# Performance work log

Hardware: AMD Instinct MI355X
Metric: run time of the kernel (lower is better)

## Reference

```python
import jax, jax.numpy as jnp
import numpy as np

B, S, HID = 1, 2048, 4096
NH, NKV, HD = 32, 8, 128
WINDOW = 1024
ROPE_THETA = 1e6
NEG = -1e9


def rotate_half(x):
    x1, x2 = jnp.split(x, 2, axis=-1)
    return jnp.concatenate((-x2, x1), axis=-1)


def setup_inputs() -> dict:
    key = jax.random.key(0)
    ks = jax.random.split(key, 10)
    hidden_states = jax.random.normal(ks[0], (B, S, HID), jnp.float32)
    # rotary tables [max_pos, head_dim]
    inv_freq = 1.0 / (ROPE_THETA ** (jnp.arange(0, HD, 2, dtype=jnp.float32) / HD))
    t = jnp.arange(S, dtype=jnp.float32)
    freqs = jnp.outer(t, inv_freq)                       # [S, HD/2]
    emb = jnp.concatenate((freqs, freqs), axis=-1)       # [S, HD]
    cos, sin = jnp.cos(emb), jnp.sin(emb)
    position_ids = jnp.arange(S, dtype=jnp.int64)[None, :].astype(jnp.int32)
    # sliding-window causal additive mask [B,1,S,S]
    i = jnp.arange(S)[:, None]
    j = jnp.arange(S)[None, :]
    allowed = (j <= i) & (j > i - WINDOW)
    attention_mask = jnp.where(allowed, 0.0, NEG).astype(jnp.float32)[None, None]
    sc = 0.02
    Wq = jax.random.normal(ks[1], (HID, NH * HD), jnp.float32) * sc
    bq = jax.random.normal(ks[2], (NH * HD,), jnp.float32) * sc
    Wk = jax.random.normal(ks[3], (HID, NKV * HD), jnp.float32) * sc
    bk = jax.random.normal(ks[4], (NKV * HD,), jnp.float32) * sc
    Wv = jax.random.normal(ks[5], (HID, NKV * HD), jnp.float32) * sc
    bv = jax.random.normal(ks[6], (NKV * HD,), jnp.float32) * sc
    Wo = jax.random.normal(ks[7], (NH * HD, HID), jnp.float32) * sc
    bo = jax.random.normal(ks[8], (HID,), jnp.float32) * sc
    return dict(hidden_states=hidden_states, attention_mask=attention_mask,
                position_ids=position_ids, cos=cos, sin=sin,
                Wq=Wq, bq=bq, Wk=Wk, bk=bk, Wv=Wv, bv=bv, Wo=Wo, bo=bo)


def reference(hidden_states, attention_mask, position_ids, cos, sin,
              Wq, bq, Wk, bk, Wv, bv, Wo, bo):
    bsz, q_len, _ = hidden_states.shape
    q = (hidden_states @ Wq + bq).reshape(bsz, q_len, NH, HD).transpose(0, 2, 1, 3)
    k = (hidden_states @ Wk + bk).reshape(bsz, q_len, NKV, HD).transpose(0, 2, 1, 3)
    v = (hidden_states @ Wv + bv).reshape(bsz, q_len, NKV, HD).transpose(0, 2, 1, 3)
    # RoPE: cos/sin gathered by position_ids -> [B,1,S,HD]
    c = cos[position_ids][:, None]
    s = sin[position_ids][:, None]
    q = q * c + rotate_half(q) * s
    k = k * c + rotate_half(k) * s
    # GQA repeat_kv: [B,NKV,S,HD] -> [B,NH,S,HD]
    n_rep = NH // NKV
    k = jnp.repeat(k, n_rep, axis=1)
    v = jnp.repeat(v, n_rep, axis=1)
    scores = jnp.einsum('bhqd,bhkd->bhqk', q, k) / np.sqrt(HD).astype(np.float32)
    scores = scores + attention_mask[:, :, :, :k.shape[2]]
    probs = jax.nn.softmax(scores.astype(jnp.float32), axis=-1).astype(q.dtype)
    attn = jnp.einsum('bhqk,bhkd->bhqd', probs, v)
    attn = attn.transpose(0, 2, 1, 3).reshape(bsz, q_len, NH * HD)
    return attn @ Wo + bo
```

## Files before the change

kernel.cpp:

```cpp
#include <hip/hip_runtime.h>
#include <stdint.h>

typedef unsigned short u16;
typedef __attribute__((ext_vector_type(4))) float f32x4;
typedef __attribute__((ext_vector_type(16))) float f32x16;
typedef __attribute__((ext_vector_type(8))) __bf16 bf16x8;
typedef __attribute__((ext_vector_type(4))) u16 u16x4;
typedef __attribute__((ext_vector_type(8))) u16 u16x8;
typedef __attribute__((ext_vector_type(4))) unsigned int u32x4;

#define S_LEN 2048
#define HIDDEN 4096
#define NHEAD 32
#define NKVH 8
#define HD 128
#define WIN 1024

__device__ __forceinline__ float bf2f(u16 u) {
  union { unsigned int i; float f; } x; x.i = ((unsigned int)u) << 16; return x.f;
}
__device__ __forceinline__ u16 f2bf(float f) {
  union { float f; unsigned int i; } x; x.f = f;
  unsigned int r = x.i + 0x7FFFu + ((x.i >> 16) & 1u);
  return (u16)(r >> 16);
}

__device__ __forceinline__ void gload16(const void* g, void* l) {
  __builtin_amdgcn_global_load_lds((const __attribute__((address_space(1))) void*)g,
                                   (__attribute__((address_space(3))) void*)l, 16, 0, 0);
}

__device__ __forceinline__ unsigned int cvtpk_bf16(float a, float b) {
  unsigned int w;
  asm("v_cvt_pk_bf16_f32 %0, %1, %2" : "=v"(w) : "v"(a), "v"(b));
  return w;
}

__device__ __forceinline__ void transp_f32(const float* __restrict__ in, int istride,
                                           u16* __restrict__ out, int ostride,
                                           int bx, int by, char* smem) {
  float (*tile)[68] = (float (*)[68])smem;
  int r0 = bx * 64, c0 = by * 64;
  int t = threadIdx.x;
  int tr = t >> 4;
  int tc = (t & 15) * 4;
#pragma unroll
  for (int i = 0; i < 4; ++i) {
    int r = i * 16 + tr;
    *(f32x4*)&tile[r][tc] = *(const f32x4*)(in + (size_t)(r0 + r) * istride + c0 + tc);
  }
  __syncthreads();
#pragma unroll
  for (int i = 0; i < 4; ++i) {
    int rr = i * 16 + tr;
    u16x4 o;
#pragma unroll
    for (int j = 0; j < 4; ++j) o[j] = f2bf(tile[tc + j][rr]);
    *(u16x4*)(out + (size_t)(c0 + rr) * ostride + r0 + tc) = o;
  }
}

__global__ __launch_bounds__(256) void prep_k(const float* __restrict__ X,
                                              const float* __restrict__ Wq, const float* __restrict__ Wk,
                                              const float* __restrict__ Wv,
                                              const float* __restrict__ bq, const float* __restrict__ bk,
                                              const float* __restrict__ bv,
                                              u16* __restrict__ Xb, u16* __restrict__ WT,
                                              float* __restrict__ bqkv) {
  __shared__ __align__(16) char smem[17408];
  int bid = blockIdx.x;
  if (bid < 4096) {
    size_t i = ((size_t)bid * 256 + threadIdx.x) * 8;
    f32x4 a = *(const f32x4*)(X + i);
    f32x4 b = *(const f32x4*)(X + i + 4);
    u16x8 o;
    o[0] = f2bf(a[0]); o[1] = f2bf(a[1]); o[2] = f2bf(a[2]); o[3] = f2bf(a[3]);
    o[4] = f2bf(b[0]); o[5] = f2bf(b[1]); o[6] = f2bf(b[2]); o[7] = f2bf(b[3]);
    *(u16x8*)(Xb + i) = o;
  } else if (bid < 8192) {
    int tt = bid - 4096;
    transp_f32(Wq, 4096, WT, 4096, tt & 63, tt >> 6, smem);
  } else if (bid < 9216) {
    int tt = bid - 8192;
    transp_f32(Wk, 1024, WT + (size_t)4096 * 4096, 4096, tt & 63, tt >> 6, smem);
  } else if (bid < 10240) {
    int tt = bid - 9216;
    transp_f32(Wv, 1024, WT + (size_t)5120 * 4096, 4096, tt & 63, tt >> 6, smem);
  } else {
    int i = (bid - 10240) * 256 + threadIdx.x;
    float v = (i < 4096) ? bq[i] : (i < 5120 ? bk[i - 4096] : bv[i - 5120]);
    bqkv[i] = v;
  }
}

__global__ __launch_bounds__(512, 2) void gemmqkv_k(const u16* __restrict__ A, const u16* __restrict__ Bt,
                                                    const float* __restrict__ bias,
                                                    const int* __restrict__ pos,
                                                    const float* __restrict__ cosT, const float* __restrict__ sinT,
                                                    u16* __restrict__ Q, u16* __restrict__ Kf,
                                                    u16* __restrict__ Vf, int K) {
  __shared__ __align__(16) u16 SM[49152];
  u16* SA = SM;
  u16* SB = SM + 24576;

  int tid = threadIdx.x;
  int w = tid >> 6, l = tid & 63;
  int cl = l & 15, g = l >> 4;
  int wr = w >> 2, wc = w & 3;

  int cpx = gridDim.x >> 3;
  int wg = (blockIdx.x & 7) * cpx + (blockIdx.x >> 3);
  int bm = wg & 7, bn = wg >> 3;

  const u16* Ag = A + (size_t)(bm * 256) * K;
  const u16* Bg = Bt + (size_t)(bn * 256) * K;
  int srow = w * 16 + (l >> 2);
  int csrc = ((l & 3) ^ ((l >> 3) & 3)) * 8;
  int rdc = (g ^ ((cl >> 1) & 3)) << 3;

  f32x4 acc[8][4] = {};
  int NT = K >> 5;

  auto stage = [&](int slot, int tt, int u) {
    if (u < 2) {
      gload16(Ag + (size_t)(u * 128 + srow) * K + tt * 32 + csrc,
              (void*)(SA + slot * 8192 + u * 4096 + w * 512));
    } else {
      int ub = u - 2;
      gload16(Bg + (size_t)(ub * 128 + srow) * K + tt * 32 + csrc,
              (void*)(SB + slot * 8192 + ub * 4096 + w * 512));
    }
  };

#pragma unroll
  for (int u = 0; u < 4; ++u) stage(0, 0, u);
#pragma unroll
  for (int u = 0; u < 4; ++u) stage(1, 1, u);

  for (int t = 0; t < NT; ++t) {
    asm volatile("s_waitcnt vmcnt(4)" ::: "memory");
    __builtin_amdgcn_s_barrier();
    asm volatile("" ::: "memory");

    int slot = t % 3, ss = (t + 2) % 3;
    int ts = t + 2; if (ts >= NT) ts -= NT;
#pragma unroll
    for (int u = 0; u < 4; ++u) stage(ss, ts, u);

    const u16* sa = SA + slot * 8192;
    const u16* sb = SB + slot * 8192;
    bf16x8 af[8], bf[4];
#pragma unroll
    for (int mi = 0; mi < 8; ++mi)
      af[mi] = *(const bf16x8*)(sa + (wr * 128 + mi * 16 + cl) * 32 + rdc);
#pragma unroll
    for (int ni = 0; ni < 4; ++ni)
      bf[ni] = *(const bf16x8*)(sb + (wc * 64 + ni * 16 + cl) * 32 + rdc);
    __builtin_amdgcn_s_setprio(1);
#pragma unroll
    for (int mi = 0; mi < 8; ++mi)
#pragma unroll
      for (int ni = 0; ni < 4; ++ni)
        acc[mi][ni] = __builtin_amdgcn_mfma_f32_16x16x32_bf16(af[mi], bf[ni], acc[mi][ni], 0, 0, 0);
    __builtin_amdgcn_s_setprio(0);
  }

  asm volatile("s_waitcnt vmcnt(0)" ::: "memory");
  __syncthreads();

  u16 (*tileL)[264] = (u16 (*)[264])SM;
  const float qs = 0.08838834764831845f;
#pragma unroll
  for (int hp = 0; hp < 2; ++hp) {
    if (wr == hp) {
#pragma unroll
      for (int mi = 0; mi < 8; ++mi)
#pragma unroll
        for (int ni = 0; ni < 4; ++ni) {
          int col = wc * 64 + ni * 16 + cl;
          float bb = bias[bn * 256 + col];
#pragma unroll
          for (int r = 0; r < 4; ++r)
            tileL[mi * 16 + g * 4 + r][col] = f2bf(acc[mi][ni][r] + bb);
        }
    }
    __syncthreads();

    int s0 = bm * 256 + hp * 128;
    if (bn < 16) {
      int r = tid >> 2, u2 = tid & 3;
      int hl = u2 >> 1, u = u2 & 1;
      int hq = bn * 2 + hl;
      int s = s0 + r;
      int ps = pos[s];
      const float* cb = cosT + (size_t)ps * 128;
      const float* sb = sinT + (size_t)ps * 128;
      u16* dst = Q + ((size_t)hq * S_LEN + s) * HD;
#pragma unroll
      for (int c8 = 0; c8 < 4; ++c8) {
        int d0 = u * 32 + c8 * 8;
        u16x8 xlo = *(const u16x8*)&tileL[r][hl * 128 + d0];
        u16x8 xhi = *(const u16x8*)&tileL[r][hl * 128 + d0 + 64];
        u16x8 lo, hi;
#pragma unroll
        for (int j = 0; j < 8; ++j) {
          int d = d0 + j;
          float x0 = bf2f(xlo[j]);
          float x1 = bf2f(xhi[j]);
          lo[j] = f2bf((x0 * cb[d] - x1 * sb[d]) * qs);
          hi[j] = f2bf((x1 * cb[d + 64] + x0 * sb[d + 64]) * qs);
        }
        *(u16x8*)(dst + d0) = lo;
        *(u16x8*)(dst + d0 + 64) = hi;
      }
    } else if (bn < 20) {
      int r = tid >> 2, u2 = tid & 3;
      int hl = u2 >> 1, u = u2 & 1;
      int kh = (bn - 16) * 2 + hl;
      int s = s0 + r;
      int ps = pos[s];
      const float* cb = cosT + (size_t)ps * 128;
      const float* sb = sinT + (size_t)ps * 128;
      int t2 = s >> 5, cr = s & 31;
#pragma unroll
      for (int c8 = 0; c8 < 4; ++c8) {
        int d0 = u * 32 + c8 * 8;
        u16x8 xlo = *(const u16x8*)&tileL[r][hl * 128 + d0];
        u16x8 xhi = *(const u16x8*)&tileL[r][hl * 128 + d0 + 64];
        u16x8 lo, hi;
#pragma unroll
        for (int j = 0; j < 8; ++j) {
          int d = d0 + j;
          float x0 = bf2f(xlo[j]);
          float x1 = bf2f(xhi[j]);
          lo[j] = f2bf(x0 * cb[d] - x1 * sb[d]);
          hi[j] = f2bf(x1 * cb[d + 64] + x0 * sb[d + 64]);
        }
        size_t base_lo = ((size_t)(kh * 64 + t2) * 8 + (d0 >> 4)) * 512 + (size_t)(cr + 32 * ((d0 >> 3) & 1)) * 8;
        *(u16x8*)(Kf + base_lo) = lo;
        int dh = d0 + 64;
        size_t base_hi = ((size_t)(kh * 64 + t2) * 8 + (dh >> 4)) * 512 + (size_t)(cr + 32 * ((dh >> 3) & 1)) * 8;
        *(u16x8*)(Kf + base_hi) = hi;
      }
    } else {
#pragma unroll
      for (int i = 0; i < 8; ++i) {
        int c = i * 512 + tid;
        int lv = c & 63, sl = (c >> 6) & 1, dt = (c >> 7) & 3;
        int t_local = (c >> 9) & 3, hl = c >> 11;
        int kh = (bn - 20) * 2 + hl;
        int rl = t_local * 32 + sl * 16 + (lv >> 5) * 8;
        int colv = hl * 128 + dt * 32 + (lv & 31);
        u16x8 o;
#pragma unroll
        for (int j = 0; j < 8; ++j) o[j] = tileL[rl + j][colv];
        int tglob = bm * 8 + hp * 4 + t_local;
        size_t addr = ((size_t)(kh * 512 + tglob * 8 + dt * 2 + sl)) * 512 + (size_t)lv * 8;
        *(u16x8*)(Vf + addr) = o;
      }
    }
    __syncthreads();
  }
}

template <int BM, int BN, int MINW, typename TOUT>
__global__ __launch_bounds__(256, MINW) void gemm4_k(const u16* __restrict__ A, const u16* __restrict__ Bt,
                                                     const float* __restrict__ bias, TOUT* __restrict__ C,
                                                     int M, int N, int K) {
  constexpr int WM = BM / 2, WN = BN / 2;
  constexpr int MRA = WM / 16, MRB = WN / 16;
  constexpr int NA = BM / 64, NB = BN / 64;
  constexpr int NL = NA + NB;
  __shared__ __align__(16) u16 SA[3 * BM * 32];
  __shared__ __align__(16) u16 SB[3 * BN * 32];

  int tid = threadIdx.x;
  int w = tid >> 6, l = tid & 63;
  int cl = l & 15, g = l >> 4;
  int wr = w >> 1, wc = w & 1;

  int cpx = gridDim.x >> 3;
  int wg = (blockIdx.x & 7) * cpx + (blockIdx.x >> 3);
  int nbm = M / BM;
  int bm = wg % nbm, bn = wg / nbm;

  const u16* Ag = A + (size_t)(bm * BM) * K;
  const u16* Bg = Bt + (size_t)(bn * BN) * K;
  int srow = w * 16 + (l >> 2);
  int csrc = ((l & 3) ^ ((l >> 3) & 3)) * 8;
  int rdc = (g ^ ((cl >> 1) & 3)) << 3;

  f32x4 acc[MRA][MRB] = {};
  int NT = K >> 5;

  auto stage = [&](int slot, int tt, int h) {
    if (h < NA) {
      gload16(Ag + (size_t)(h * 64 + srow) * K + tt * 32 + csrc,
              (void*)(SA + slot * (BM * 32) + (h * 64 + w * 16) * 32));
    } else {
      int hb = h - NA;
      gload16(Bg + (size_t)(hb * 64 + srow) * K + tt * 32 + csrc,
              (void*)(SB + slot * (BN * 32) + (hb * 64 + w * 16) * 32));
    }
  };

#pragma unroll
  for (int h = 0; h < NL; ++h) stage(0, 0, h);
#pragma unroll
  for (int h = 0; h < NL; ++h) stage(1, 1, h);

  for (int t = 0; t < NT; ++t) {
    if constexpr (NL == 5) asm volatile("s_waitcnt vmcnt(5)" ::: "memory");
    else if constexpr (NL == 4) asm volatile("s_waitcnt vmcnt(4)" ::: "memory");
    else asm volatile("s_waitcnt vmcnt(3)" ::: "memory");
    __builtin_amdgcn_s_barrier();
    asm volatile("" ::: "memory");

    int slot = t % 3, ss = (t + 2) % 3;
    int ts = t + 2; if (ts >= NT) ts -= NT;
#pragma unroll
    for (int h = 0; h < NL; ++h) stage(ss, ts, h);

    const u16* sa = SA + slot * (BM * 32);
    const u16* sb = SB + slot * (BN * 32);
    bf16x8 af[MRA], bf[MRB];
#pragma unroll
    for (int mi = 0; mi < MRA; ++mi)
      af[mi] = *(const bf16x8*)(sa + (wr * WM + mi * 16 + cl) * 32 + rdc);
#pragma unroll
    for (int ni = 0; ni < MRB; ++ni)
      bf[ni] = *(const bf16x8*)(sb + (wc * WN + ni * 16 + cl) * 32 + rdc);
    __builtin_amdgcn_s_setprio(1);
#pragma unroll
    for (int mi = 0; mi < MRA; ++mi)
#pragma unroll
      for (int ni = 0; ni < MRB; ++ni)
        acc[mi][ni] = __builtin_amdgcn_mfma_f32_16x16x32_bf16(af[mi], bf[ni], acc[mi][ni], 0, 0, 0);
    __builtin_amdgcn_s_setprio(0);
  }

  asm volatile("s_waitcnt vmcnt(0)" ::: "memory");

#pragma unroll
  for (int mi = 0; mi < MRA; ++mi) {
    int row0 = bm * BM + wr * WM + mi * 16 + g * 4;
#pragma unroll
    for (int ni = 0; ni < MRB; ++ni) {
      int col = bn * BN + wc * WN + ni * 16 + cl;
      float bb = bias[col];
      f32x4 a = acc[mi][ni];
#pragma unroll
      for (int r = 0; r < 4; ++r) {
        float v = a[r] + bb;
        if constexpr (sizeof(TOUT) == 2) C[(size_t)(row0 + r) * N + col] = f2bf(v);
        else C[(size_t)(row0 + r) * N + col] = v;
      }
    }
  }
}

__global__ __launch_bounds__(256, 2) void attnwot_k(const u16* __restrict__ Q, const u16* __restrict__ Kf,
                                                    const u16* __restrict__ Vf, u16* __restrict__ O,
                                                    const float* __restrict__ Wo, u16* __restrict__ WT) {
  __shared__ __align__(16) char smem[17408];
  if (blockIdx.x >= 512) {
    int tt = blockIdx.x - 512;
    transp_f32(Wo, 4096, WT, 4096, tt & 63, tt >> 6, smem);
    return;
  }
  int l = threadIdx.x & 63, w = threadIdx.x >> 6;
  int col = l & 31, hi = l >> 5;
  int bid = blockIdx.x;
  int kh = bid & 7;
  int head = (bid >> 3) & 3;
  int qbp = bid >> 5;
  int qb = (qbp & 1) ? (15 - (qbp >> 1)) : (qbp >> 1);
  int h = kh * 4 + head;
  int q0 = qb * 128 + w * 32;

  bf16x8 qf[8];
  const u16* qbase = Q + ((size_t)h * S_LEN + q0 + col) * HD + hi * 8;
#pragma unroll
  for (int ks = 0; ks < 8; ++ks) qf[ks] = *(const bf16x8*)(qbase + ks * 16);

  f32x16 ot[4];
#pragma unroll
  for (int dt = 0; dt < 4; ++dt)
#pragma unroll
    for (int r = 0; r < 16; ++r) ot[dt][r] = 0.f;
  float m_r = -3.0e38f, l_r = 0.f;

  const u16* kf0 = Kf + (size_t)kh * 64 * 4096 + (size_t)l * 8;
  const u16* vf0 = Vf + (size_t)kh * 512 * 512 + (size_t)l * 8;

  int jstart = q0 >= WIN ? q0 - WIN : 0;
  bf16x8 kfr[8];
  {
    const u16* kb = kf0 + (size_t)(jstart >> 5) * 4096;
#pragma unroll
    for (int ks = 0; ks < 8; ++ks) kfr[ks] = *(const bf16x8*)(kb + ks * 512);
  }

  for (int j0 = jstart; j0 <= q0; j0 += 32) {
    int t = j0 >> 5;
    f32x16 sA = {}, sB = {};
#pragma unroll
    for (int ks = 0; ks < 4; ++ks)
      sA = __builtin_amdgcn_mfma_f32_32x32x16_bf16(kfr[ks], qf[ks], sA, 0, 0, 0);
#pragma unroll
    for (int ks = 4; ks < 8; ++ks)
      sB = __builtin_amdgcn_mfma_f32_32x32x16_bf16(kfr[ks], qf[ks], sB, 0, 0, 0);
    int tn = (j0 + 32 <= q0) ? (t + 1) : t;
    const u16* kbn = kf0 + (size_t)tn * 4096;
    bf16x8 kfn[8];
#pragma unroll
    for (int ks = 0; ks < 8; ++ks) kfn[ks] = *(const bf16x8*)(kbn + ks * 512);
    const u16* vb = vf0 + (size_t)t * 4096;
    bf16x8 vfr[8];
#pragma unroll
    for (int c = 0; c < 8; ++c) vfr[c] = *(const bf16x8*)(vb + c * 512);

    f32x16 s = sA + sB;

    if (j0 + 31 > q0 || j0 < q0 - 992) {
      int q = q0 + col;
#pragma unroll
      for (int r = 0; r < 16; ++r) {
        int kv = j0 + (r & 3) + 8 * (r >> 2) + 4 * hi;
        if (kv > q || kv <= q - WIN) s[r] = -3.0e38f;
      }
    }
    float vm = fmaxf(fmaxf(fmaxf(s[0], s[1]), fmaxf(s[2], s[3])),
                     fmaxf(fmaxf(s[4], s[5]), fmaxf(s[6], s[7])));
    vm = fmaxf(vm, fmaxf(fmaxf(fmaxf(s[8], s[9]), fmaxf(s[10], s[11])),
                         fmaxf(fmaxf(s[12], s[13]), fmaxf(s[14], s[15]))));
    vm = fmaxf(vm, __shfl_xor(vm, 32));
    float mnew = fmaxf(m_r, vm);
    float sc = __expf(m_r - mnew);
    m_r = mnew;
    float rs = 0.f;
#pragma unroll
    for (int r = 0; r < 16; ++r) {
      float pv = __expf(s[r] - mnew);
      s[r] = pv;
      rs += pv;
    }
    rs += __shfl_xor(rs, 32);
    l_r = l_r * sc + rs;
#pragma unroll
    for (int dt = 0; dt < 4; ++dt)
#pragma unroll
      for (int r = 0; r < 16; ++r) ot[dt][r] *= sc;

    bf16x8 pb[2];
#pragma unroll
    for (int sl = 0; sl < 2; ++sl) {
      int b = sl * 8;
      unsigned int a0 = cvtpk_bf16(s[b + 0], s[b + 1]);
      unsigned int c0 = cvtpk_bf16(s[b + 4], s[b + 5]);
      asm("v_permlane32_swap_b32 %0, %1" : "+v"(a0), "+v"(c0));
      unsigned int a1 = cvtpk_bf16(s[b + 2], s[b + 3]);
      unsigned int c1 = cvtpk_bf16(s[b + 6], s[b + 7]);
      asm("v_permlane32_swap_b32 %0, %1" : "+v"(a1), "+v"(c1));
      u32x4 pv = {a0, a1, c0, c1};
      pb[sl] = __builtin_bit_cast(bf16x8, pv);
    }
#pragma unroll
    for (int dt = 0; dt < 4; ++dt) {
      ot[dt] = __builtin_amdgcn_mfma_f32_32x32x16_bf16(vfr[dt * 2 + 0], pb[0], ot[dt], 0, 0, 0);
      ot[dt] = __builtin_amdgcn_mfma_f32_32x32x16_bf16(vfr[dt * 2 + 1], pb[1], ot[dt], 0, 0, 0);
    }
#pragma unroll
    for (int ks = 0; ks < 8; ++ks) kfr[ks] = kfn[ks];
  }

  float inv = 1.0f / l_r;
#pragma unroll
  for (int dt = 0; dt < 4; ++dt) {
#pragma unroll
    for (int g2 = 0; g2 < 4; ++g2) {
      u16x4 o;
#pragma unroll
      for (int i = 0; i < 4; ++i) o[i] = f2bf(ot[dt][g2 * 4 + i] * inv);
      *(u16x4*)(O + (size_t)(q0 + col) * HIDDEN + h * HD + dt * 32 + g2 * 8 + hi * 4) = o;
    }
  }
}

extern "C" void kernel_launch(void* const* d_in, const int* in_sizes, int n_in,
                              void* d_out, int out_size, void* d_ws, size_t ws_size,
                              hipStream_t stream) {
  const float* X = (const float*)d_in[0];
  const int* pos = (const int*)d_in[2];
  const float* cosT = (const float*)d_in[3];
  const float* sinT = (const float*)d_in[4];
  const float* Wq = (const float*)d_in[5];
  const float* bq = (const float*)d_in[6];
  const float* Wk = (const float*)d_in[7];
  const float* bk = (const float*)d_in[8];
  const float* Wv = (const float*)d_in[9];
  const float* bv = (const float*)d_in[10];
  const float* Wo = (const float*)d_in[11];
  const float* bo = (const float*)d_in[12];
  float* out = (float*)d_out;

  const size_t MB = 1ull << 20;
  char* ws = (char*)d_ws;
  u16* WT = (u16*)ws;
  u16* Xb = (u16*)(ws + 48 * MB);
  u16* attnO = Xb;
  u16* Qs = (u16*)(ws + 64 * MB);
  u16* Kfr = (u16*)(ws + 88 * MB);
  u16* Vfr = (u16*)(ws + 92 * MB);
  float* bqkv = (float*)(ws + 96 * MB);

  prep_k<<<10264, 256, 0, stream>>>(X, Wq, Wk, Wv, bq, bk, bv, Xb, WT, bqkv);

  gemmqkv_k<<<192, 512, 0, stream>>>(Xb, WT, bqkv, pos, cosT, sinT, Qs, Kfr, Vfr, 4096);

  attnwot_k<<<4608, 256, 0, stream>>>(Qs, Kfr, Vfr, attnO, Wo, WT);

  gemm4_k<128, 128, 3, float><<<512, 256, 0, stream>>>(attnO, WT, bo, out, 2048, 4096, 4096);
}
```

Measured before the change: 301.1 us.

## Retile QKV GEMM to 128x384 blocks for 256-block grid

The fused QKV projection GEMM moves from 256x256 tiles (192 blocks) to 128x384 tiles (256 blocks), so the grid matches the 256 compute units on MI355X and avoids a partial second wave. Each warp now computes a 4x6 MFMA fragment grid instead of 8x4. The epilogue is restructured so every tile handles three 128-wide head slices, each of which can be Q, K or V, with RoPE and layout writes adjusted to match. Each block loads more B data per unit of A, which lowers arithmetic intensity per block and changes LDS usage.

Result: faster. 286.8 us (median of 2 runs) (-4.7%).

```diff
diff --git a/kernel.cpp b/kernel.cpp
--- a/kernel.cpp
+++ b/kernel.cpp
@@ -101,7 +101,7 @@
                                                     u16* __restrict__ Vf, int K) {
   __shared__ __align__(16) u16 SM[49152];
   u16* SA = SM;
-  u16* SB = SM + 24576;
+  u16* SB = SM + 12288;
 
   int tid = threadIdx.x;
   int w = tid >> 6, l = tid & 63;
@@ -110,25 +110,25 @@
 
   int cpx = gridDim.x >> 3;
   int wg = (blockIdx.x & 7) * cpx + (blockIdx.x >> 3);
-  int bm = wg & 7, bn = wg >> 3;
-
-  const u16* Ag = A + (size_t)(bm * 256) * K;
-  const u16* Bg = Bt + (size_t)(bn * 256) * K;
+  int bm = wg & 15, bn = wg >> 4;
+
+  const u16* Ag = A + (size_t)(bm * 128) * K;
+  const u16* Bg = Bt + (size_t)(bn * 384) * K;
   int srow = w * 16 + (l >> 2);
   int csrc = ((l & 3) ^ ((l >> 3) & 3)) * 8;
   int rdc = (g ^ ((cl >> 1) & 3)) << 3;
 
-  f32x4 acc[8][4] = {};
+  f32x4 acc[4][6] = {};
   int NT = K >> 5;
 
   auto stage = [&](int slot, int tt, int u) {
-    if (u < 2) {
-      gload16(Ag + (size_t)(u * 128 + srow) * K + tt * 32 + csrc,
-              (void*)(SA + slot * 8192 + u * 4096 + w * 512));
+    if (u == 0) {
+      gload16(Ag + (size_t)srow * K + tt * 32 + csrc,
+              (void*)(SA + slot * 4096 + w * 512));
     } else {
-      int ub = u - 2;
+      int ub = u - 1;
       gload16(Bg + (size_t)(ub * 128 + srow) * K + tt * 32 + csrc,
-              (void*)(SB + slot * 8192 + ub * 4096 + w * 512));
+              (void*)(SB + slot * 12288 + ub * 4096 + w * 512));
     }
   };
 
@@ -147,20 +147,20 @@
 #pragma unroll
     for (int u = 0; u < 4; ++u) stage(ss, ts, u);
 
-    const u16* sa = SA + slot * 8192;
-    const u16* sb = SB + slot * 8192;
-    bf16x8 af[8], bf[4];
-#pragma unroll
-    for (int mi = 0; mi < 8; ++mi)
-      af[mi] = *(const bf16x8*)(sa + (wr * 128 + mi * 16 + cl) * 32 + rdc);
-#pragma unroll
-    for (int ni = 0; ni < 4; ++ni)
-      bf[ni] = *(const bf16x8*)(sb + (wc * 64 + ni * 16 + cl) * 32 + rdc);
+    const u16* sa = SA + slot * 4096;
+    const u16* sb = SB + slot * 12288;
+    bf16x8 af[4], bf[6];
+#pragma unroll
+    for (int mi = 0; mi < 4; ++mi)
+      af[mi] = *(const bf16x8*)(sa + (wr * 64 + mi * 16 + cl) * 32 + rdc);
+#pragma unroll
+    for (int ni = 0; ni < 6; ++ni)
+      bf[ni] = *(const bf16x8*)(sb + (wc * 96 + ni * 16 + cl) * 32 + rdc);
     __builtin_amdgcn_s_setprio(1);
 #pragma unroll
-    for (int mi = 0; mi < 8; ++mi)
-#pragma unroll
-      for (int ni = 0; ni < 4; ++ni)
+    for (int mi = 0; mi < 4; ++mi)
+#pragma unroll
+      for (int ni = 0; ni < 6; ++ni)
         acc[mi][ni] = __builtin_amdgcn_mfma_f32_16x16x32_bf16(af[mi], bf[ni], acc[mi][ni], 0, 0, 0);
     __builtin_amdgcn_s_setprio(0);
   }
@@ -168,17 +168,17 @@
   asm volatile("s_waitcnt vmcnt(0)" ::: "memory");
   __syncthreads();
 
-  u16 (*tileL)[264] = (u16 (*)[264])SM;
+  u16 (*tileL)[392] = (u16 (*)[392])SM;
   const float qs = 0.08838834764831845f;
 #pragma unroll
   for (int hp = 0; hp < 2; ++hp) {
     if (wr == hp) {
 #pragma unroll
-      for (int mi = 0; mi < 8; ++mi)
-#pragma unroll
-        for (int ni = 0; ni < 4; ++ni) {
-          int col = wc * 64 + ni * 16 + cl;
-          float bb = bias[bn * 256 + col];
+      for (int mi = 0; mi < 4; ++mi)
+#pragma unroll
+        for (int ni = 0; ni < 6; ++ni) {
+          int col = wc * 96 + ni * 16 + cl;
+          float bb = bias[bn * 384 + col];
 #pragma unroll
           for (int r = 0; r < 4; ++r)
             tileL[mi * 16 + g * 4 + r][col] = f2bf(acc[mi][ni][r] + bb);
@@ -186,19 +186,19 @@
     }
     __syncthreads();
 
-    int s0 = bm * 256 + hp * 128;
-    if (bn < 16) {
-      int r = tid >> 2, u2 = tid & 3;
-      int hl = u2 >> 1, u = u2 & 1;
-      int hq = bn * 2 + hl;
-      int s = s0 + r;
-      int ps = pos[s];
-      const float* cb = cosT + (size_t)ps * 128;
-      const float* sb = sinT + (size_t)ps * 128;
-      u16* dst = Q + ((size_t)hq * S_LEN + s) * HD;
-#pragma unroll
-      for (int c8 = 0; c8 < 4; ++c8) {
-        int d0 = u * 32 + c8 * 8;
+    int s0 = bm * 128 + hp * 64;
+#pragma unroll
+    for (int hl = 0; hl < 3; ++hl) {
+      int c0 = bn * 384 + hl * 128;
+      int hidx = c0 >> 7;
+      if (hidx < 32) {
+        int r = tid >> 3, u = tid & 7;
+        int s = s0 + r;
+        int ps = pos[s];
+        const float* cb = cosT + (size_t)ps * 128;
+        const float* sb = sinT + (size_t)ps * 128;
+        u16* dst = Q + ((size_t)hidx * S_LEN + s) * HD;
+        int d0 = u * 8;
         u16x8 xlo = *(const u16x8*)&tileL[r][hl * 128 + d0];
         u16x8 xhi = *(const u16x8*)&tileL[r][hl * 128 + d0 + 64];
         u16x8 lo, hi;
@@ -212,19 +212,15 @@
         }
         *(u16x8*)(dst + d0) = lo;
         *(u16x8*)(dst + d0 + 64) = hi;
-      }
-    } else if (bn < 20) {
-      int r = tid >> 2, u2 = tid & 3;
-      int hl = u2 >> 1, u = u2 & 1;
-      int kh = (bn - 16) * 2 + hl;
-      int s = s0 + r;
-      int ps = pos[s];
-      const float* cb = cosT + (size_t)ps * 128;
-      const float* sb = sinT + (size_t)ps * 128;
-      int t2 = s >> 5, cr = s & 31;
-#pragma unroll
-      for (int c8 = 0; c8 < 4; ++c8) {
-        int d0 = u * 32 + c8 * 8;
+      } else if (hidx < 40) {
+        int kh = hidx - 32;
+        int r = tid >> 3, u = tid & 7;
+        int s = s0 + r;
+        int ps = pos[s];
+        const float* cb = cosT + (size_t)ps * 128;
+        const float* sb = sinT + (size_t)ps * 128;
+        int t2 = s >> 5, cr = s & 31;
+        int d0 = u * 8;
         u16x8 xlo = *(const u16x8*)&tileL[r][hl * 128 + d0];
         u16x8 xhi = *(const u16x8*)&tileL[r][hl * 128 + d0 + 64];
         u16x8 lo, hi;
@@ -241,22 +237,21 @@
         int dh = d0 + 64;
         size_t base_hi = ((size_t)(kh * 64 + t2) * 8 + (dh >> 4)) * 512 + (size_t)(cr + 32 * ((dh >> 3) & 1)) * 8;
         *(u16x8*)(Kf + base_hi) = hi;
-      }
-    } else {
-#pragma unroll
-      for (int i = 0; i < 8; ++i) {
-        int c = i * 512 + tid;
-        int lv = c & 63, sl = (c >> 6) & 1, dt = (c >> 7) & 3;
-        int t_local = (c >> 9) & 3, hl = c >> 11;
-        int kh = (bn - 20) * 2 + hl;
-        int rl = t_local * 32 + sl * 16 + (lv >> 5) * 8;
-        int colv = hl * 128 + dt * 32 + (lv & 31);
-        u16x8 o;
-#pragma unroll
-        for (int j = 0; j < 8; ++j) o[j] = tileL[rl + j][colv];
-        int tglob = bm * 8 + hp * 4 + t_local;
-        size_t addr = ((size_t)(kh * 512 + tglob * 8 + dt * 2 + sl)) * 512 + (size_t)lv * 8;
-        *(u16x8*)(Vf + addr) = o;
+      } else {
+        int kh = hidx - 40;
+#pragma unroll
+        for (int i = 0; i < 2; ++i) {
+          int c = i * 512 + tid;
+          int lv = c & 63, sl = (c >> 6) & 1, dt = (c >> 7) & 3, t_local = (c >> 9) & 1;
+          int rl = t_local * 32 + sl * 16 + (lv >> 5) * 8;
+          int colv = hl * 128 + dt * 32 + (lv & 31);
+          u16x8 o;
+#pragma unroll
+          for (int j = 0; j < 8; ++j) o[j] = tileL[rl + j][colv];
+          int tglob = bm * 4 + hp * 2 + t_local;
+          size_t addr = ((size_t)(kh * 512 + tglob * 8 + dt * 2 + sl)) * 512 + (size_t)lv * 8;
+          *(u16x8*)(Vf + addr) = o;
+        }
       }
     }
     __syncthreads();
@@ -516,7 +511,7 @@
 
   prep_k<<<10264, 256, 0, stream>>>(X, Wq, Wk, Wv, bq, bk, bv, Xb, WT, bqkv);
 
-  gemmqkv_k<<<192, 512, 0, stream>>>(Xb, WT, bqkv, pos, cosT, sinT, Qs, Kfr, Vfr, 4096);
+  gemmqkv_k<<<256, 512, 0, stream>>>(Xb, WT, bqkv, pos, cosT, sinT, Qs, Kfr, Vfr, 4096);
 
   attnwot_k<<<4608, 256, 0, stream>>>(Qs, Kfr, Vfr, attnO, Wo, WT);
 
```
